# Kernel optimization log

Measured on AMD Instinct MI355X. Metric: run time of the kernel, lower is better.

Reference implementation:

```python
import jax, jax.numpy as jnp
import numpy as np

B, T, H, M = 16, 1024, 512, 80
NHEADS, HDIM = 8, H // 8


def _p(key, shape, scale=0.05):
    return scale * jax.random.normal(key, shape, dtype=jnp.float32)


def setup_inputs() -> dict:
    key = jax.random.key(0)
    ks = jax.random.split(key, 20)
    return {
        "encoder_memory": jax.random.normal(ks[0], (B, T, H), dtype=jnp.float32),
        "target_mel": jax.random.normal(ks[1], (B, T, M), dtype=jnp.float32),
        # prenet Linear(mel_dim -> hidden_dim)
        "w_prenet": _p(ks[2], (H, M)), "b_prenet": _p(ks[3], (H,)),
        # MultiheadAttention packed in-proj (3H, H) and out-proj (H, H)
        "in_proj_w": _p(ks[4], (3 * H, H)), "in_proj_b": _p(ks[5], (3 * H,)),
        "out_proj_w": _p(ks[6], (H, H)), "out_proj_b": _p(ks[7], (H,)),
        # 2-layer LSTM (torch gate order i,f,g,o); h0=c0=0 each step so W_hh acts on zeros
        "w_ih0": _p(ks[8], (4 * H, 2 * H)), "w_hh0": _p(ks[9], (4 * H, H)),
        "b_ih0": _p(ks[10], (4 * H,)), "b_hh0": _p(ks[11], (4 * H,)),
        "w_ih1": _p(ks[12], (4 * H, H)), "w_hh1": _p(ks[13], (4 * H, H)),
        "b_ih1": _p(ks[14], (4 * H,)), "b_hh1": _p(ks[15], (4 * H,)),
        # mel projection Linear(hidden_dim -> mel_dim)
        "w_mel": _p(ks[16], (M, H)), "b_mel": _p(ks[17], (M,)),
    }


def _lstm_cell_zero_state(x, w_ih, w_hh, b_ih, b_hh):
    # single step from zero (h, c): the W_hh @ h0 term is exactly zero
    gates = x @ w_ih.T + (b_ih + b_hh)  # (B,T,4H)
    i, f, g, o = jnp.split(gates, 4, axis=-1)
    c = jax.nn.sigmoid(i) * jnp.tanh(g)  # f * c_prev == 0
    return jax.nn.sigmoid(o) * jnp.tanh(c)


def reference(encoder_memory, target_mel, w_prenet, b_prenet,
              in_proj_w, in_proj_b, out_proj_w, out_proj_b,
              w_ih0, w_hh0, b_ih0, b_hh0, w_ih1, w_hh1, b_ih1, b_hh1,
              w_mel, b_mel):
    # teacher forcing: prev_mel at step t is zeros (t=0) else target_mel[:, t-1]
    prev = jnp.concatenate(
        [jnp.zeros((B, 1, M), dtype=target_mel.dtype), target_mel[:, :-1]], axis=1)
    pre = jax.nn.relu(prev @ w_prenet.T + b_prenet)  # (B,T,H); dropout is identity (eval)

    # cross-attention: each step's length-1 query attends over all encoder frames,
    # which vectorizes to standard (no-mask) MHA with queries = pre
    wq, wk, wv = jnp.split(in_proj_w, 3, axis=0)
    bq, bk, bv = jnp.split(in_proj_b, 3, axis=0)
    q = (pre @ wq.T + bq).reshape(B, T, NHEADS, HDIM)
    k = (encoder_memory @ wk.T + bk).reshape(B, T, NHEADS, HDIM)
    v = (encoder_memory @ wv.T + bv).reshape(B, T, NHEADS, HDIM)
    scale = 1.0 / jnp.sqrt(jnp.float32(HDIM))
    scores = jnp.einsum('bqhd,bkhd->bhqk', q * scale, k)  # (B,8,T,T)
    attn = jax.nn.softmax(scores, axis=-1)
    ctx = jnp.einsum('bhqk,bkhd->bqhd', attn, v).reshape(B, T, H)
    attn_out = ctx @ out_proj_w.T + out_proj_b  # (B,T,H)

    dec_in = jnp.concatenate([pre, attn_out], axis=-1)  # (B,T,2H)
    h1 = _lstm_cell_zero_state(dec_in, w_ih0, w_hh0, b_ih0, b_hh0)
    h2 = _lstm_cell_zero_state(h1, w_ih1, w_hh1, b_ih1, b_hh1)
    return h2 @ w_mel.T + b_mel  # (B,T,M)
```

## Files before the change

kernel.cpp:

```cpp
#include <hip/hip_runtime.h>


typedef _Float16 f16;
typedef _Float16 f16x8 __attribute__((ext_vector_type(8)));
typedef _Float16 f16x4 __attribute__((ext_vector_type(4)));
typedef float f32x4 __attribute__((ext_vector_type(4)));

constexpr int B_ = 16, T_ = 1024, H_ = 512, M_ = 80;
constexpr int NH_ = 8, D_ = 64;
constexpr int N_ = B_ * T_;

#define MFMA16(a, b, c) __builtin_amdgcn_mfma_f32_16x16x32_f16(a, b, c, 0, 0, 0)

__device__ __forceinline__ void gload_lds16(const f16* g, f16* l) {
  __builtin_amdgcn_global_load_lds(
      (const __attribute__((address_space(1))) void*)g,
      (__attribute__((address_space(3))) void*)l, 16, 0, 0);
}

__device__ __forceinline__ float fexp2(float x) {
#if __has_builtin(__builtin_amdgcn_exp2f)
  return __builtin_amdgcn_exp2f(x);
#else
  return exp2f(x);
#endif
}

template <int EPI, bool CONCATA, bool NCHK>
__device__ __forceinline__ void mgemm_body(
    const f16* __restrict__ A, const f16* __restrict__ A2,
    const f16* __restrict__ Wt, const float* __restrict__ bias,
    const float* __restrict__ bias2, float scale, void* __restrict__ outp,
    int K, int N, int r0, int c0, f16* As, f16* Bs) {
  const int tid = threadIdx.x;
  const int lane = tid & 63, wid = tid >> 6;
  const int lq = lane & 15, lg = lane >> 4;
  const int wm = wid >> 1, wn = wid & 1;

  f32x4 acc[4][4] = {};

  for (int k0 = 0; k0 < K; k0 += 64) {
#pragma unroll
    for (int it = 0; it < 4; ++it) {
      const int off = it * 4096 + wid * 1024 + lane * 16;
      const int row = off >> 7;
      const int cb = (off >> 4) & 7;
      const int kc = k0 + ((cb ^ (row & 7)) << 3);
      const f16* src;
      if (CONCATA) {
        src = (kc < 512) ? (A + (size_t)(r0 + row) * 512 + kc)
                         : (A2 + (size_t)(r0 + row) * 512 + (kc - 512));
      } else {
        src = A + (size_t)(r0 + row) * K + kc;
      }
      gload_lds16(src, (f16*)((char*)As + off));
    }
#pragma unroll
    for (int it = 0; it < 4; ++it) {
      const int off = it * 4096 + wid * 1024 + lane * 16;
      const int row = off >> 7;
      const int cb = (off >> 4) & 7;
      int crow = c0 + row;
      if (NCHK) crow = crow < N ? crow : N - 1;
      gload_lds16(Wt + (size_t)crow * K + k0 + ((cb ^ (row & 7)) << 3),
                  (f16*)((char*)Bs + off));
    }
    __syncthreads();
#pragma unroll
    for (int kk = 0; kk < 2; ++kk) {
      f16x8 af[4], bf[4];
#pragma unroll
      for (int m = 0; m < 4; ++m) {
        const int row = wm * 64 + m * 16 + lq;
        af[m] = *(const f16x8*)((const char*)As + row * 128 +
                                (((kk * 4 + lg) ^ (row & 7)) << 4));
      }
#pragma unroll
      for (int n = 0; n < 4; ++n) {
        const int row = wn * 64 + n * 16 + lq;
        bf[n] = *(const f16x8*)((const char*)Bs + row * 128 +
                                (((kk * 4 + lg) ^ (row & 7)) << 4));
      }
#pragma unroll
      for (int m = 0; m < 4; ++m)
#pragma unroll
        for (int n = 0; n < 4; ++n) acc[m][n] = MFMA16(af[m], bf[n], acc[m][n]);
    }
    __syncthreads();
  }

#pragma unroll
  for (int m = 0; m < 4; ++m) {
    const int rbase = r0 + wm * 64 + m * 16 + lg * 4;
#pragma unroll
    for (int n = 0; n < 4; ++n) {
      const int col = c0 + wn * 64 + n * 16 + lq;
      if (NCHK && col >= N) continue;
      const float bsum = bias[col] + (bias2 ? bias2[col] : 0.f);
      const f32x4 a = acc[m][n];
#pragma unroll
      for (int r = 0; r < 4; ++r) {
        const int row = rbase + r;
        float v = (a[r] + bsum) * scale;
        if (EPI == 1) v = fmaxf(v, 0.f);
        if (EPI == 4)
          ((float*)outp)[(size_t)row * N + col] = v;
        else
          ((f16*)outp)[(size_t)row * N + col] = (f16)v;
      }
    }
  }
}

template <int EPI, bool CONCATA, bool NCHK>
__global__ __launch_bounds__(256) void mgemm(
    const f16* __restrict__ A, const f16* __restrict__ A2,
    const f16* __restrict__ Wt, const float* __restrict__ bias,
    const float* __restrict__ bias2, float scale, void* __restrict__ outp,
    int K, int N) {
  __shared__ f16 As[128 * 64];
  __shared__ f16 Bs[128 * 64];
  mgemm_body<EPI, CONCATA, NCHK>(A, A2, Wt, bias, bias2, scale, outp, K, N,
                                 blockIdx.x * 128, blockIdx.y * 128, As, Bs);
}

__device__ __forceinline__ void kv_body(const f16* __restrict__ A,
                                        const f16* __restrict__ Wt,
                                        const float* __restrict__ bias,
                                        f16* __restrict__ kout,
                                        f16* __restrict__ vout, int r0, int c0,
                                        f16* As, f16 (*Bs)[128 * 64]) {
  constexpr int K = 512;
  const int tid = threadIdx.x;
  const int lane = tid & 63, wid = tid >> 6;
  const int lq = lane & 15, lg = lane >> 4;
  const int wm = wid >> 1, wn = wid & 1;

  f32x4 acc[2][4][4] = {};

  for (int k0 = 0; k0 < K; k0 += 64) {
#pragma unroll
    for (int it = 0; it < 4; ++it) {
      const int off = it * 4096 + tid * 16;
      const int row = off >> 7;
      const int cb = (off >> 4) & 7;
      const int kc = k0 + ((cb ^ (row & 7)) << 3);
      gload_lds16(A + (size_t)(r0 + row) * K + kc, (f16*)((char*)As + off));
    }
#pragma unroll
    for (int g = 0; g < 2; ++g) {
#pragma unroll
      for (int it = 0; it < 4; ++it) {
        const int off = it * 4096 + tid * 16;
        const int row = off >> 7;
        const int cb = (off >> 4) & 7;
        gload_lds16(
            Wt + (size_t)(g * 512 + c0 + row) * K + k0 + ((cb ^ (row & 7)) << 3),
            (f16*)((char*)&Bs[g][0] + off));
      }
    }
    __syncthreads();
#pragma unroll
    for (int kk = 0; kk < 2; ++kk) {
      f16x8 af[4];
#pragma unroll
      for (int m = 0; m < 4; ++m) {
        const int row = wm * 64 + m * 16 + lq;
        af[m] = *(const f16x8*)((const char*)As + row * 128 +
                                (((kk * 4 + lg) ^ (row & 7)) << 4));
      }
#pragma unroll
      for (int g = 0; g < 2; ++g)
#pragma unroll
        for (int n = 0; n < 4; ++n) {
          const int row = wn * 64 + n * 16 + lq;
          const f16x8 bf = *(const f16x8*)((const char*)&Bs[g][0] + row * 128 +
                                           (((kk * 4 + lg) ^ (row & 7)) << 4));
#pragma unroll
          for (int m = 0; m < 4; ++m)
            acc[g][m][n] = MFMA16(af[m], bf, acc[g][m][n]);
        }
    }
    __syncthreads();
  }

#pragma unroll
  for (int m = 0; m < 4; ++m) {
    const int rbase = r0 + wm * 64 + m * 16 + lg * 4;
    const int b = rbase >> 10, t = rbase & (T_ - 1);
#pragma unroll
    for (int n = 0; n < 4; ++n) {
      const int col = c0 + wn * 64 + n * 16 + lq;
      const float bk = bias[col];
#pragma unroll
      for (int r = 0; r < 4; ++r)
        kout[(size_t)(rbase + r) * 512 + col] = (f16)(acc[0][m][n][r] + bk);
      const float bv = bias[512 + col];
      const int head = col >> 6, d = col & 63;
      f16x4 pk;
#pragma unroll
      for (int r = 0; r < 4; ++r) pk[r] = (f16)(acc[1][m][n][r] + bv);
      *(f16x4*)(vout + ((size_t)((b * NH_ + head) * D_ + d)) * T_ + t) = pk;
    }
  }
}

__global__ __launch_bounds__(256, 2) void prenet_kv(
    const f16* __restrict__ PM, const f16* __restrict__ WP,
    const float* __restrict__ bpre, f16* __restrict__ pre,
    const f16* __restrict__ EncB, const f16* __restrict__ Wkv,
    const float* __restrict__ bkv, f16* __restrict__ kout,
    f16* __restrict__ vout) {
  __shared__ f16 As[128 * 64];
  __shared__ f16 Bs[2][128 * 64];
  const int bid = blockIdx.x;
  const int f = bid >> 1;
  const int r0 = (f >> 2) * 128, c0 = (f & 3) * 128;
  if (bid & 1) {
    kv_body(EncB, Wkv, bkv, kout, vout, r0, c0, As, Bs);
  } else {
    mgemm_body<1, false, false>(PM, nullptr, WP, bpre, nullptr, 1.f, pre, 128,
                                512, r0, c0, As, &Bs[0][0]);
  }
}

template <bool CONCATA>
__global__ __launch_bounds__(256, 2) void lstm_fused(
    const f16* __restrict__ A, const f16* __restrict__ A2,
    const f16* __restrict__ Wih, const float* __restrict__ bih,
    const float* __restrict__ bhh, f16* __restrict__ Hout_) {
  constexpr int K = CONCATA ? 1024 : 512;
  __shared__ f16 As[128 * 64];
  __shared__ f16 Bs[3][128 * 64];
  const int tid = threadIdx.x;
  const int lane = tid & 63, wid = tid >> 6;
  const int lq = lane & 15, lg = lane >> 4;
  const int wm = wid >> 1, wn = wid & 1;
  const int r0 = blockIdx.x * 128, c0 = blockIdx.y * 128;

  f32x4 acc[3][4][4] = {};

  for (int k0 = 0; k0 < K; k0 += 64) {
#pragma unroll
    for (int it = 0; it < 4; ++it) {
      const int off = it * 4096 + tid * 16;
      const int row = off >> 7;
      const int cb = (off >> 4) & 7;
      const int kc = k0 + ((cb ^ (row & 7)) << 3);
      const f16* src;
      if (CONCATA) {
        src = (kc < 512) ? (A + (size_t)(r0 + row) * 512 + kc)
                         : (A2 + (size_t)(r0 + row) * 512 + (kc - 512));
      } else {
        src = A + (size_t)(r0 + row) * K + kc;
      }
      gload_lds16(src, (f16*)((char*)As + off));
    }
#pragma unroll
    for (int g = 0; g < 3; ++g) {
      const int gbase = (g == 0) ? 0 : 512 * (g + 1);
#pragma unroll
      for (int it = 0; it < 4; ++it) {
        const int off = it * 4096 + tid * 16;
        const int row = off >> 7;
        const int cb = (off >> 4) & 7;
        gload_lds16(
            Wih + (size_t)(gbase + c0 + row) * K + k0 + ((cb ^ (row & 7)) << 3),
            (f16*)((char*)&Bs[g][0] + off));
      }
    }
    __syncthreads();
#pragma unroll
    for (int kk = 0; kk < 2; ++kk) {
      f16x8 af[4];
#pragma unroll
      for (int m = 0; m < 4; ++m) {
        const int row = wm * 64 + m * 16 + lq;
        af[m] = *(const f16x8*)((const char*)As + row * 128 +
                                (((kk * 4 + lg) ^ (row & 7)) << 4));
      }
#pragma unroll
      for (int g = 0; g < 3; ++g)
#pragma unroll
        for (int n = 0; n < 4; ++n) {
          const int row = wn * 64 + n * 16 + lq;
          const f16x8 bf = *(const f16x8*)((const char*)&Bs[g][0] + row * 128 +
                                           (((kk * 4 + lg) ^ (row & 7)) << 4));
#pragma unroll
          for (int m = 0; m < 4; ++m)
            acc[g][m][n] = MFMA16(af[m], bf, acc[g][m][n]);
        }
    }
    __syncthreads();
  }

#pragma unroll
  for (int n = 0; n < 4; ++n) {
    const int c = c0 + wn * 64 + n * 16 + lq;
    const float bi = bih[c] + bhh[c];
    const float bg = bih[1024 + c] + bhh[1024 + c];
    const float bo = bih[1536 + c] + bhh[1536 + c];
#pragma unroll
    for (int m = 0; m < 4; ++m) {
      const int rbase = r0 + wm * 64 + m * 16 + lg * 4;
#pragma unroll
      for (int r = 0; r < 4; ++r) {
        const float gi = acc[0][m][n][r] + bi;
        const float gg = acc[1][m][n][r] + bg;
        const float go = acc[2][m][n][r] + bo;
        const float si = 1.f / (1.f + __expf(-gi));
        const float so = 1.f / (1.f + __expf(-go));
        const float tg = 2.f / (1.f + __expf(-2.f * gg)) - 1.f;
        const float cc = si * tg;
        const float tc = 2.f / (1.f + __expf(-2.f * cc)) - 1.f;
        Hout_[(size_t)(rbase + r) * 512 + c] = (f16)(so * tc);
      }
    }
  }
}

__global__ __launch_bounds__(256, 4) void attn_mfma7(
    const f16* __restrict__ q, const f16* __restrict__ k,
    const f16* __restrict__ vT, f16* __restrict__ ctx) {
  __shared__ f16 Ks[2][64 * 64];
  __shared__ f16 Vs[2][64 * 64];
  __shared__ f16 Ps[4][16 * 64];
  const int bid = blockIdx.x;
  const int nid = (bid & 7) * 128 + (bid >> 3);
  const int qt = nid & 7, bh = nid >> 3;
  const int head = bh & 7, b = bh >> 3;
  const int tid = threadIdx.x, lane = tid & 63, wid = tid >> 6;
  const int lq = lane & 15, lg = lane >> 4;

  const f16* kbase = k + ((size_t)b * T_) * H_ + head * D_;
  const f16* vbase = vT + (size_t)bh * D_ * T_;

  auto stage = [&](int kt, int buf) {
#pragma unroll
    for (int it = 0; it < 2; ++it) {
      const int off = it * 4096 + tid * 16;
      const int row = off >> 7;
      const int sc = ((((off >> 4) & 7) ^ (row & 7)) << 3);
      gload_lds16(kbase + (size_t)(kt * 64 + row) * H_ + sc,
                  (f16*)((char*)&Ks[buf][0] + off));
      gload_lds16(vbase + (size_t)row * T_ + kt * 64 + sc,
                  (f16*)((char*)&Vs[buf][0] + off));
    }
  };

  const int q0 = qt * 128 + wid * 32;
  f16x8 qf[2][2];
#pragma unroll
  for (int s = 0; s < 2; ++s)
#pragma unroll
    for (int kk = 0; kk < 2; ++kk)
      qf[s][kk] = *(const f16x8*)(q + ((size_t)(b * T_) + q0 + s * 16 + lq) * H_ +
                                  head * D_ + kk * 32 + lg * 8);

  f16x8 ones;
#pragma unroll
  for (int j = 0; j < 8; ++j) ones[j] = (f16)1.f;

  f32x4 accO[2][4] = {};
  f32x4 accL[2] = {};
  char* pw = (char*)&Ps[wid][0] + lq * 128;
  const int psw = (lq & 7) << 4;

  stage(0, 0);
  __syncthreads();

  for (int kt = 0; kt < T_ / 64; ++kt) {
    const int cur = kt & 1;
    if (kt < T_ / 64 - 1) stage(kt + 1, cur ^ 1);

    f16x8 kf[4][2];
#pragma unroll
    for (int n = 0; n < 4; ++n)
#pragma unroll
      for (int kk = 0; kk < 2; ++kk) {
        const int row = n * 16 + lq;
        kf[n][kk] = *(const f16x8*)((const char*)&Ks[cur][0] + row * 128 +
                                    (((kk * 4 + lg) ^ (row & 7)) << 4));
      }

#pragma unroll
    for (int s = 0; s < 2; ++s) {
      f32x4 ssw[4] = {};
      __builtin_amdgcn_s_setprio(1);
#pragma unroll
      for (int n = 0; n < 4; ++n)
#pragma unroll
        for (int kk = 0; kk < 2; ++kk)
          ssw[n] = MFMA16(kf[n][kk], qf[s][kk], ssw[n]);
      __builtin_amdgcn_s_setprio(0);

#pragma unroll
      for (int n = 0; n < 4; ++n) {
        f16x4 pk;
#pragma unroll
        for (int r = 0; r < 4; ++r) pk[r] = (f16)fexp2(ssw[n][r]);
        *(f16x4*)(pw + ((n * 32 + lg * 8) ^ psw)) = pk;
      }
      f16x8 pb[2];
#pragma unroll
      for (int kk = 0; kk < 2; ++kk)
        pb[kk] = *(const f16x8*)(pw + ((((kk * 4 + lg) << 4)) ^ psw));

      __builtin_amdgcn_s_setprio(1);
#pragma unroll
      for (int kk = 0; kk < 2; ++kk)
        accL[s] = MFMA16(ones, pb[kk], accL[s]);
#pragma unroll
      for (int n = 0; n < 4; ++n) {
        const int row = n * 16 + lq;
#pragma unroll
        for (int kk = 0; kk < 2; ++kk) {
          const f16x8 vf =
              *(const f16x8*)((const char*)&Vs[cur][0] + row * 128 +
                              (((kk * 4 + lg) ^ (row & 7)) << 4));
          accO[s][n] = MFMA16(vf, pb[kk], accO[s][n]);
        }
      }
      __builtin_amdgcn_s_setprio(0);
    }
    __syncthreads();
  }

#pragma unroll
  for (int s = 0; s < 2; ++s) {
    const float inv = 1.f / accL[s][0];
    const size_t rowoff = ((size_t)(b * T_) + q0 + s * 16 + lq) * H_ + head * D_;
#pragma unroll
    for (int n = 0; n < 4; ++n) {
      f16x4 o;
#pragma unroll
      for (int r = 0; r < 4; ++r) o[r] = (f16)(accO[s][n][r] * inv);
      *(f16x4*)(ctx + rowoff + n * 16 + lg * 4) = o;
    }
  }
}

constexpr int C0 = 2097152;
constexpr int C1 = C0 + 196608;
constexpr int C2 = C1 + 65536;
constexpr int C3 = C2 + 524288;
constexpr int C4 = C3 + 262144;
constexpr int C5 = C4 + 10240;
constexpr int C6 = C5 + 524288;
constexpr int C7 = C6 + 16384;
__global__ void conv_all(const float* __restrict__ enc, const float* __restrict__ inw,
                         const float* __restrict__ outw, const float* __restrict__ wih0,
                         const float* __restrict__ wih1, const float* __restrict__ wmel,
                         const float* __restrict__ tmel, const float* __restrict__ wpre,
                         f16* denc, f16* dinw, f16* doutw, f16* dwih0,
                         f16* dwih1, f16* dwmel, f16* dpm, f16* dwp) {
  const int i = blockIdx.x * blockDim.x + threadIdx.x;
  if (i >= C7) return;
  if (i < C5) {
    const float* s;
    f16* d;
    int off;
    if (i < C0) { s = enc; d = denc; off = i; }
    else if (i < C1) { s = inw; d = dinw; off = i - C0; }
    else if (i < C2) { s = outw; d = doutw; off = i - C1; }
    else if (i < C3) { s = wih0; d = dwih0; off = i - C2; }
    else if (i < C4) { s = wih1; d = dwih1; off = i - C3; }
    else { s = wmel; d = dwmel; off = i - C4; }
    const float4 v = ((const float4*)s)[off];
    f16x4 o = {(f16)v.x, (f16)v.y, (f16)v.z, (f16)v.w};
    ((f16x4*)d)[off] = o;
  } else if (i < C6) {
    const int j = i - C5;
    const int r = j >> 5, c4 = (j & 31) * 4;
    const int t = r & (T_ - 1);
    f16x4 o = {};
    if (t != 0 && c4 < M_) {
      const float4 v = *(const float4*)(tmel + (size_t)(r - 1) * M_ + c4);
      o = {(f16)v.x, (f16)v.y, (f16)v.z, (f16)v.w};
    }
    *(f16x4*)(dpm + (size_t)r * 128 + c4) = o;
  } else {
    const int j = i - C6;
    const int r = j >> 5, c4 = (j & 31) * 4;
    f16x4 o = {};
    if (c4 < M_) {
      const float4 v = *(const float4*)(wpre + (size_t)r * M_ + c4);
      o = {(f16)v.x, (f16)v.y, (f16)v.z, (f16)v.w};
    }
    *(f16x4*)(dwp + (size_t)r * 128 + c4) = o;
  }
}

extern "C" void kernel_launch(void* const* d_in, const int* in_sizes, int n_in,
                              void* d_out, int out_size, void* d_ws,
                              size_t ws_size, hipStream_t stream) {
  const float* enc = (const float*)d_in[0];
  const float* tmel = (const float*)d_in[1];
  const float* w_pre = (const float*)d_in[2];
  const float* b_pre = (const float*)d_in[3];
  const float* inw = (const float*)d_in[4];
  const float* inb = (const float*)d_in[5];
  const float* outw = (const float*)d_in[6];
  const float* outb = (const float*)d_in[7];
  const float* wih0 = (const float*)d_in[8];
  const float* bih0 = (const float*)d_in[10];
  const float* bhh0 = (const float*)d_in[11];
  const float* wih1 = (const float*)d_in[12];
  const float* bih1 = (const float*)d_in[14];
  const float* bhh1 = (const float*)d_in[15];
  const float* wmel = (const float*)d_in[16];
  const float* bmel = (const float*)d_in[17];

  f16* wsh = (f16*)d_ws;
  const size_t SEG = (size_t)N_ * H_;
  f16* EncB = wsh;
  f16* h1 = wsh + SEG;
  f16* pre = wsh + 2 * SEG;
  f16* qb = wsh + 3 * SEG;
  f16* kbuf = wsh + 4 * SEG;
  f16* vTb = wsh + 5 * SEG;
  f16* ctx = wsh + 6 * SEG;
  f16* aout = EncB;
  f16* h2 = qb;
  f16* WP = wsh + 7 * SEG;
  f16* WIN = WP + 512 * 128;
  f16* WOUT = WIN + 1536 * 512;
  f16* WIH0 = WOUT + 512 * 512;
  f16* WIH1 = WIH0 + (size_t)2048 * 1024;
  f16* WMEL = WIH1 + 2048 * 512;
  f16* PM = WMEL + 80 * 512;

  const dim3 blk(256);
  conv_all<<<(C7 + 255) / 256, blk, 0, stream>>>(
      enc, inw, outw, wih0, wih1, wmel, tmel, w_pre, EncB, WIN, WOUT, WIH0,
      WIH1, WMEL, PM, WP);

  prenet_kv<<<dim3(1024), blk, 0, stream>>>(PM, WP, b_pre, pre, EncB,
                                            WIN + 512 * 512, inb + 512, kbuf,
                                            vTb);

  const dim3 g512(N_ / 128, 4), g80(N_ / 128, 1);
  mgemm<0, false, false><<<g512, blk, 0, stream>>>(
      pre, nullptr, WIN, inb, nullptr, 0.125f * 1.44269504088896f, qb, 512, 512);
  attn_mfma7<<<dim3(1024), blk, 0, stream>>>(qb, kbuf, vTb, ctx);
  mgemm<0, false, false><<<g512, blk, 0, stream>>>(ctx, nullptr, WOUT, outb,
                                                   nullptr, 1.f, aout, 512, 512);
  lstm_fused<true><<<g512, blk, 0, stream>>>(pre, aout, WIH0, bih0, bhh0, h1);
  lstm_fused<false><<<g512, blk, 0, stream>>>(h1, nullptr, WIH1, bih1, bhh1, h2);
  mgemm<4, false, true><<<g80, blk, 0, stream>>>(h2, nullptr, WMEL, bmel,
                                                 nullptr, 1.f, (float*)d_out,
                                                 512, 80);
}
```

Baseline: 264.3 us.

## Double-buffer LDS tiles in fused LSTM GEMM with K-step of 32

Reworks the fused LSTM gate GEMM main loop to use two LDS buffers with a K-step of 32 instead of a single buffer with K-step 64. The global-to-LDS load for the next K slice is issued before computing on the current slice, so load latency can overlap the MFMA work, and one barrier per iteration is dropped. LDS footprint stays the same, but there are twice as many iterations and a different XOR swizzle for the narrower rows, which could change bank-conflict behaviour.

```diff
diff --git a/kernel.cpp b/kernel.cpp
--- a/kernel.cpp
+++ b/kernel.cpp
@@ -230,8 +230,9 @@
     const f16* __restrict__ Wih, const float* __restrict__ bih,
     const float* __restrict__ bhh, f16* __restrict__ Hout_) {
   constexpr int K = CONCATA ? 1024 : 512;
-  __shared__ f16 As[128 * 64];
-  __shared__ f16 Bs[3][128 * 64];
+  constexpr int NS = K / 32;
+  __shared__ f16 As[2][128 * 32];
+  __shared__ f16 Bs[2][3][128 * 32];
   const int tid = threadIdx.x;
   const int lane = tid & 63, wid = tid >> 6;
   const int lq = lane & 15, lg = lane >> 4;
@@ -240,13 +241,13 @@
 
   f32x4 acc[3][4][4] = {};
 
-  for (int k0 = 0; k0 < K; k0 += 64) {
-#pragma unroll
-    for (int it = 0; it < 4; ++it) {
+  auto stage = [&](int ks, int buf) {
+#pragma unroll
+    for (int it = 0; it < 2; ++it) {
       const int off = it * 4096 + tid * 16;
-      const int row = off >> 7;
-      const int cb = (off >> 4) & 7;
-      const int kc = k0 + ((cb ^ (row & 7)) << 3);
+      const int row = off >> 6;
+      const int cb = (off >> 4) & 3;
+      const int kc = ks * 32 + ((cb ^ ((row >> 1) & 3)) << 3);
       const f16* src;
       if (CONCATA) {
         src = (kc < 512) ? (A + (size_t)(r0 + row) * 512 + kc)
@@ -254,43 +255,49 @@
       } else {
         src = A + (size_t)(r0 + row) * K + kc;
       }
-      gload_lds16(src, (f16*)((char*)As + off));
+      gload_lds16(src, (f16*)((char*)&As[buf][0] + off));
     }
 #pragma unroll
     for (int g = 0; g < 3; ++g) {
       const int gbase = (g == 0) ? 0 : 512 * (g + 1);
 #pragma unroll
-      for (int it = 0; it < 4; ++it) {
+      for (int it = 0; it < 2; ++it) {
         const int off = it * 4096 + tid * 16;
-        const int row = off >> 7;
-        const int cb = (off >> 4) & 7;
-        gload_lds16(
-            Wih + (size_t)(gbase + c0 + row) * K + k0 + ((cb ^ (row & 7)) << 3),
-            (f16*)((char*)&Bs[g][0] + off));
-      }
-    }
-    __syncthreads();
-#pragma unroll
-    for (int kk = 0; kk < 2; ++kk) {
-      f16x8 af[4];
-#pragma unroll
-      for (int m = 0; m < 4; ++m) {
-        const int row = wm * 64 + m * 16 + lq;
-        af[m] = *(const f16x8*)((const char*)As + row * 128 +
-                                (((kk * 4 + lg) ^ (row & 7)) << 4));
-      }
-#pragma unroll
-      for (int g = 0; g < 3; ++g)
-#pragma unroll
-        for (int n = 0; n < 4; ++n) {
-          const int row = wn * 64 + n * 16 + lq;
-          const f16x8 bf = *(const f16x8*)((const char*)&Bs[g][0] + row * 128 +
-                                           (((kk * 4 + lg) ^ (row & 7)) << 4));
-#pragma unroll
-          for (int m = 0; m < 4; ++m)
-            acc[g][m][n] = MFMA16(af[m], bf, acc[g][m][n]);
-        }
-    }
+        const int row = off >> 6;
+        const int cb = (off >> 4) & 3;
+        const int kc = ks * 32 + ((cb ^ ((row >> 1) & 3)) << 3);
+        gload_lds16(Wih + (size_t)(gbase + c0 + row) * K + kc,
+                    (f16*)((char*)&Bs[buf][g][0] + off));
+      }
+    }
+  };
+
+  stage(0, 0);
+  __syncthreads();
+
+  for (int ks = 0; ks < NS; ++ks) {
+    const int cur = ks & 1;
+    if (ks + 1 < NS) stage(ks + 1, cur ^ 1);
+
+    f16x8 af[4];
+#pragma unroll
+    for (int m = 0; m < 4; ++m) {
+      const int row = wm * 64 + m * 16 + lq;
+      af[m] = *(const f16x8*)((const char*)&As[cur][0] + row * 64 +
+                              ((lg ^ ((row >> 1) & 3)) << 4));
+    }
+#pragma unroll
+    for (int g = 0; g < 3; ++g)
+#pragma unroll
+      for (int n = 0; n < 4; ++n) {
+        const int row = wn * 64 + n * 16 + lq;
+        const f16x8 bf =
+            *(const f16x8*)((const char*)&Bs[cur][g][0] + row * 64 +
+                            ((lg ^ ((row >> 1) & 3)) << 4));
+#pragma unroll
+        for (int m = 0; m < 4; ++m)
+          acc[g][m][n] = MFMA16(af[m], bf, acc[g][m][n]);
+      }
     __syncthreads();
   }
 
```

After: 272.8 us. 3.2% more time.
